# Kernel tuning notes

Hardware: AMD Instinct MI355X
Metric: run time of the kernel (lower is better)

The kernel has to match this reference:

```python
import jax, jax.numpy as jnp
import numpy as np

N = 100000          # num nodes
E = 1_600_000       # num edges
D = 128             # in_channels
H = 128             # hidden_channels
NUM_LAYERS = 3


def setup_inputs() -> dict:
    key = jax.random.key(0)
    ks = jax.random.split(key, 6)
    return {
        "emb": jax.random.normal(ks[0], (N, D), dtype=jnp.float32),
        "w1": jax.random.normal(ks[1], (H, D), dtype=jnp.float32) / np.sqrt(D).astype(np.float32),
        "b1": jnp.zeros((H,), jnp.float32),
        "w2": jax.random.normal(ks[2], (H, H), dtype=jnp.float32) / np.sqrt(H).astype(np.float32),
        "b2": jnp.zeros((H,), jnp.float32),
        "eps": jnp.zeros((NUM_LAYERS,), jnp.float32),  # learn_eps=True, init 0 per layer
        "edge_w": jax.random.uniform(ks[3], (E,), dtype=jnp.float32),
        "src": jax.random.randint(ks[4], (E,), 0, N, dtype=jnp.int32),
        "dst": jax.random.randint(ks[5], (E,), 0, N, dtype=jnp.int32),
    }


def _gin_layer(x, src, dst, edge_w, deg_inv, eps, W, b):
    # DGL GINConv(mean, edge_weight): msg = x[src] * w ; agg = mean over in-edges (divide by in-degree)
    msg = x[src] * edge_w[:, None]                                  # [E, d]
    agg = jax.ops.segment_sum(msg, dst, num_segments=N) * deg_inv[:, None]
    return ((1.0 + eps) * x + agg) @ W.T + b


def reference(emb, w1, b1, w2, b2, eps, edge_w, src, dst):
    # in-degree (count of in-edges), zero-degree nodes get 0 aggregation
    deg = jax.ops.segment_sum(jnp.ones((E,), jnp.float32), dst, num_segments=N)
    deg_inv = jnp.where(deg > 0, 1.0 / jnp.maximum(deg, 1.0), 0.0)

    x = _gin_layer(emb, src, dst, edge_w, deg_inv, eps[0], w1, b1)
    x = jax.nn.relu(x)  # dropout is identity in eval mode
    for i in range(1, NUM_LAYERS - 1):
        x = _gin_layer(x, src, dst, edge_w, deg_inv, eps[i], w2, b2)  # lin2 shared
        x = jax.nn.relu(x)
    x = _gin_layer(x, src, dst, edge_w, deg_inv, eps[NUM_LAYERS - 1], w2, b2)
    x = x.at[0].set(jnp.zeros((x.shape[1],), x.dtype))  # x[0] = zeros
    return x
```

## Files before the change

### kernel.cpp

```cpp
#include <hip/hip_runtime.h>
#include <hip/hip_bf16.h>

#define N_NODES 100000
#define N_EDGES 1600000
#define DIM 128
#define SCAN_CHUNK 1024

typedef __attribute__((ext_vector_type(8))) short bf16x8;
typedef __attribute__((ext_vector_type(4))) float f32x4;
typedef __attribute__((ext_vector_type(4))) short bf16x4;

__global__ void cvt_kernel(const float* __restrict__ in, __hip_bfloat16* __restrict__ out, int n4) {
    int i = blockIdx.x * blockDim.x + threadIdx.x;
    if (i < n4) {
        f32x4 v = ((const f32x4*)in)[i];
        bf16x4 o;
        o.x = (short)__bfloat16_as_ushort(__float2bfloat16(v.x));
        o.y = (short)__bfloat16_as_ushort(__float2bfloat16(v.y));
        o.z = (short)__bfloat16_as_ushort(__float2bfloat16(v.z));
        o.w = (short)__bfloat16_as_ushort(__float2bfloat16(v.w));
        ((bf16x4*)out)[i] = o;
    }
}

__global__ void cvtw_kernel(const float* __restrict__ w1, const float* __restrict__ w2,
                            __hip_bfloat16* __restrict__ w1b, __hip_bfloat16* __restrict__ w2b) {
    int i = blockIdx.x * blockDim.x + threadIdx.x;
    if (i < DIM * DIM) {
        w1b[i] = __float2bfloat16(w1[i]);
        w2b[i] = __float2bfloat16(w2[i]);
    }
}

#define DR_UNROLL 8
__global__ void degrank_kernel(const int* __restrict__ dst, int* __restrict__ deg,
                               int* __restrict__ rank) {
    int tid = blockIdx.x * blockDim.x + threadIdx.x;
    int nthreads = gridDim.x * blockDim.x;
    int d_[DR_UNROLL], r_[DR_UNROLL];
#pragma unroll
    for (int k = 0; k < DR_UNROLL; k++) {
        int e = tid + k * nthreads;
        d_[k] = (e < N_EDGES) ? dst[e] : -1;
    }
#pragma unroll
    for (int k = 0; k < DR_UNROLL; k++)
        if (d_[k] >= 0) r_[k] = atomicAdd(&deg[d_[k]], 1);
#pragma unroll
    for (int k = 0; k < DR_UNROLL; k++) {
        int e = tid + k * nthreads;
        if (e < N_EDGES) rank[e] = r_[k];
    }
}

__global__ void scan1_kernel(const int* __restrict__ deg, int* __restrict__ bsum) {
    __shared__ int s[256];
    int t = threadIdx.x;
    int base = blockIdx.x * SCAN_CHUNK + t * 4;
    int v = 0;
    for (int k = 0; k < 4; k++) { int i = base + k; if (i < N_NODES) v += deg[i]; }
    s[t] = v;
    __syncthreads();
    for (int off = 128; off > 0; off >>= 1) { if (t < off) s[t] += s[t + off]; __syncthreads(); }
    if (t == 0) bsum[blockIdx.x] = s[0];
}

__global__ void scan2_kernel(const int* __restrict__ bsum, int* __restrict__ bscan,
                             int* __restrict__ row_start, int nb) {
    if (threadIdx.x == 0) {
        int run = 0;
        for (int b = 0; b < nb; b++) { bscan[b] = run; run += bsum[b]; }
        row_start[N_NODES] = run;
    }
}

__global__ void scan3_kernel(const int* __restrict__ deg, const int* __restrict__ bscan,
                             int* __restrict__ row_start) {
    __shared__ int s[256];
    int t = threadIdx.x;
    int base = blockIdx.x * SCAN_CHUNK + t * 4;
    int v[4]; int tot = 0;
    for (int k = 0; k < 4; k++) { int i = base + k; v[k] = (i < N_NODES) ? deg[i] : 0; tot += v[k]; }
    s[t] = tot;
    __syncthreads();
    for (int off = 1; off < 256; off <<= 1) {
        int a = (t >= off) ? s[t - off] : 0;
        __syncthreads();
        s[t] += a;
        __syncthreads();
    }
    int run = s[t] - tot + bscan[blockIdx.x];
    for (int k = 0; k < 4; k++) {
        int i = base + k;
        if (i < N_NODES) row_start[i] = run;
        run += v[k];
    }
}

#define FI_UNROLL 4
__global__ void fill_kernel(const int* __restrict__ src, const int* __restrict__ dst,
                            const float* __restrict__ ew, const int* __restrict__ rank,
                            const int* __restrict__ row_start, int2* __restrict__ sw_s) {
    int tid = blockIdx.x * blockDim.x + threadIdx.x;
    int nthreads = gridDim.x * blockDim.x;
    int d_[FI_UNROLL], r_[FI_UNROLL], s_[FI_UNROLL], w_[FI_UNROLL], rs_[FI_UNROLL];
#pragma unroll
    for (int k = 0; k < FI_UNROLL; k++) {
        int e = tid + k * nthreads;
        if (e < N_EDGES) {
            d_[k] = dst[e]; r_[k] = rank[e]; s_[k] = src[e]; w_[k] = __float_as_int(ew[e]);
        } else d_[k] = -1;
    }
#pragma unroll
    for (int k = 0; k < FI_UNROLL; k++)
        if (d_[k] >= 0) rs_[k] = row_start[d_[k]];
#pragma unroll
    for (int k = 0; k < FI_UNROLL; k++)
        if (d_[k] >= 0) sw_s[rs_[k] + r_[k]] = make_int2(s_[k], w_[k]);
}

__global__ __launch_bounds__(256) void agg_kernel(const __hip_bfloat16* __restrict__ x,
                                                  const int* __restrict__ row_start,
                                                  const int2* __restrict__ sw_s,
                                                  const float* __restrict__ eps, int li,
                                                  __hip_bfloat16* __restrict__ h) {
    __shared__ int2 s_sw[4][64];
    int wv = threadIdx.x >> 6;
    int lane = threadIdx.x & 63;
    int n = blockIdx.x * 4 + wv;
    if (n >= N_NODES) return;
    int beg = row_start[n], end = row_start[n + 1];
    const __hip_bfloat162* xp = (const __hip_bfloat162*)x;
    float ax = 0.f, ay = 0.f;
    for (int base = beg; base < end; base += 64) {
        int cnt = min(64, end - base);
        if (lane < cnt) s_sw[wv][lane] = sw_s[base + lane];
        asm volatile("s_waitcnt lgkmcnt(0)" ::: "memory");
        int i = 0;
        for (; i + 4 <= cnt; i += 4) {
            int2 e0 = s_sw[wv][i], e1 = s_sw[wv][i + 1], e2 = s_sw[wv][i + 2], e3 = s_sw[wv][i + 3];
            __hip_bfloat162 v0 = xp[(size_t)e0.x * 64 + lane];
            __hip_bfloat162 v1 = xp[(size_t)e1.x * 64 + lane];
            __hip_bfloat162 v2 = xp[(size_t)e2.x * 64 + lane];
            __hip_bfloat162 v3 = xp[(size_t)e3.x * 64 + lane];
            float w0 = __int_as_float(e0.y), w1 = __int_as_float(e1.y);
            float w2 = __int_as_float(e2.y), w3 = __int_as_float(e3.y);
            ax += __bfloat162float(v0.x) * w0 + __bfloat162float(v1.x) * w1
                + __bfloat162float(v2.x) * w2 + __bfloat162float(v3.x) * w3;
            ay += __bfloat162float(v0.y) * w0 + __bfloat162float(v1.y) * w1
                + __bfloat162float(v2.y) * w2 + __bfloat162float(v3.y) * w3;
        }
        for (; i < cnt; i++) {
            int2 e = s_sw[wv][i];
            __hip_bfloat162 v = xp[(size_t)e.x * 64 + lane];
            float w = __int_as_float(e.y);
            ax += __bfloat162float(v.x) * w;
            ay += __bfloat162float(v.y) * w;
        }
        asm volatile("" ::: "memory");
    }
    int degn = end - beg;
    float dinv = degn > 0 ? 1.0f / (float)degn : 0.0f;
    float ep = 1.0f + eps[li];
    __hip_bfloat162 xs = xp[(size_t)n * 64 + lane];
    float vx = ep * __bfloat162float(xs.x) + ax * dinv;
    float vy = ep * __bfloat162float(xs.y) + ay * dinv;
    __hip_bfloat162 o;
    o.x = __float2bfloat16(vx);
    o.y = __float2bfloat16(vy);
    ((__hip_bfloat162*)h)[(size_t)n * 64 + lane] = o;
}

template <int RELU, int ZERO0, int OUTBF>
__global__ __launch_bounds__(256) void gemm_kernel(const __hip_bfloat16* __restrict__ A,
                                                   const __hip_bfloat16* __restrict__ W,
                                                   const float* __restrict__ bias,
                                                   void* __restrict__ outv) {
    int wave = threadIdx.x >> 6;
    int lane = threadIdx.x & 63;
    int row0 = blockIdx.x * 64 + wave * 16;
    int lr = lane & 15;
    int kg = lane >> 4;

    int arow = row0 + lr;
    if (arow > N_NODES - 1) arow = N_NODES - 1;
    const short* Ap = (const short*)A + (size_t)arow * DIM + kg * 8;
    bf16x8 a[4];
#pragma unroll
    for (int k = 0; k < 4; k++) a[k] = *(const bf16x8*)(Ap + k * 32);

    f32x4 acc[8];
#pragma unroll
    for (int jt = 0; jt < 8; jt++) {
        const short* Wp = (const short*)W + (size_t)(jt * 16 + lr) * DIM + kg * 8;
        f32x4 c = {0.f, 0.f, 0.f, 0.f};
#pragma unroll
        for (int k = 0; k < 4; k++) {
            bf16x8 b = *(const bf16x8*)(Wp + k * 32);
            c = __builtin_amdgcn_mfma_f32_16x16x32_bf16(a[k], b, c, 0, 0, 0);
        }
        acc[jt] = c;
    }

    int colb = lane & 15;
    int rb = (lane >> 4) * 4;
#pragma unroll
    for (int jt = 0; jt < 8; jt++) {
        int col = jt * 16 + colb;
        float bv = bias[col];
#pragma unroll
        for (int r = 0; r < 4; r++) {
            int grow = row0 + rb + r;
            if (grow < N_NODES) {
                float v = acc[jt][r] + bv;
                if (RELU) v = fmaxf(v, 0.f);
                if (ZERO0 && grow == 0) v = 0.f;
                if (OUTBF)
                    ((__hip_bfloat16*)outv)[(size_t)grow * DIM + col] = __float2bfloat16(v);
                else
                    ((float*)outv)[(size_t)grow * DIM + col] = v;
            }
        }
    }
}

extern "C" void kernel_launch(void* const* d_in, const int* in_sizes, int n_in,
                              void* d_out, int out_size, void* d_ws, size_t ws_size,
                              hipStream_t stream) {
    const float* emb = (const float*)d_in[0];
    const float* w1  = (const float*)d_in[1];
    const float* b1  = (const float*)d_in[2];
    const float* w2  = (const float*)d_in[3];
    const float* b2  = (const float*)d_in[4];
    const float* eps = (const float*)d_in[5];
    const float* ew  = (const float*)d_in[6];
    const int* src   = (const int*)d_in[7];
    const int* dst   = (const int*)d_in[8];
    float* out = (float*)d_out;

    char* base = (char*)d_ws;
    size_t off = 0;
    auto alloc = [&](size_t bytes) -> char* {
        char* p = base + off;
        off += (bytes + 255) & ~(size_t)255;
        return p;
    };
    int* deg            = (int*)alloc((size_t)N_NODES * 4);
    int* row_start      = (int*)alloc((size_t)(N_NODES + 1) * 4);
    int* rank           = (int*)alloc((size_t)N_EDGES * 4);
    int* bsum           = (int*)alloc(128 * 4);
    int* bscan          = (int*)alloc(128 * 4);
    int2* sw_s          = (int2*)alloc((size_t)N_EDGES * 8);
    __hip_bfloat16* h   = (__hip_bfloat16*)alloc((size_t)N_NODES * DIM * 2);
    __hip_bfloat16* xb  = (__hip_bfloat16*)alloc((size_t)N_NODES * DIM * 2);
    __hip_bfloat16* embb= (__hip_bfloat16*)alloc((size_t)N_NODES * DIM * 2);
    __hip_bfloat16* w1b = (__hip_bfloat16*)alloc(DIM * DIM * 2);
    __hip_bfloat16* w2b = (__hip_bfloat16*)alloc(DIM * DIM * 2);

    hipMemsetAsync(deg, 0, (size_t)N_NODES * 4, stream);

    cvt_kernel<<<(N_NODES * DIM / 4 + 255) / 256, 256, 0, stream>>>(emb, embb, N_NODES * DIM / 4);
    cvtw_kernel<<<(DIM * DIM + 255) / 256, 256, 0, stream>>>(w1, w2, w1b, w2b);

    {
        int nthreads = ((N_EDGES + DR_UNROLL - 1) / DR_UNROLL + 255) & ~255;
        degrank_kernel<<<nthreads / 256, 256, 0, stream>>>(dst, deg, rank);
    }
    int nb = (N_NODES + SCAN_CHUNK - 1) / SCAN_CHUNK;
    scan1_kernel<<<nb, 256, 0, stream>>>(deg, bsum);
    scan2_kernel<<<1, 64, 0, stream>>>(bsum, bscan, row_start, nb);
    scan3_kernel<<<nb, 256, 0, stream>>>(deg, bscan, row_start);
    {
        int nthreads = ((N_EDGES + FI_UNROLL - 1) / FI_UNROLL + 255) & ~255;
        fill_kernel<<<nthreads / 256, 256, 0, stream>>>(src, dst, ew, rank, row_start, sw_s);
    }

    int gemm_blocks = (N_NODES + 63) / 64;
    int agg_blocks = (N_NODES + 3) / 4;
    agg_kernel<<<agg_blocks, 256, 0, stream>>>(embb, row_start, sw_s, eps, 0, h);
    gemm_kernel<1, 0, 1><<<gemm_blocks, 256, 0, stream>>>(h, w1b, b1, xb);
    agg_kernel<<<agg_blocks, 256, 0, stream>>>(xb, row_start, sw_s, eps, 1, h);
    gemm_kernel<1, 0, 1><<<gemm_blocks, 256, 0, stream>>>(h, w2b, b2, xb);
    agg_kernel<<<agg_blocks, 256, 0, stream>>>(xb, row_start, sw_s, eps, 2, h);
    gemm_kernel<0, 1, 0><<<gemm_blocks, 256, 0, stream>>>(h, w2b, b2, out);
}
```

Before: 562.9 us.

## Fuse neighbor aggregation into MFMA GEMM via LDS-staged tiles

Each wave now aggregates 16 nodes sequentially into a swizzled LDS tile, then runs the MFMA linear layer directly from LDS. This removes the intermediate h buffer write and read and halves the kernel launches per layer. The degree/rank kernel becomes a simple grid-stride loop. The cost is far fewer concurrent waves doing gathers, which reduces latency hiding for the irregular loads.

```diff
diff --git a/kernel.cpp b/kernel.cpp
--- a/kernel.cpp
+++ b/kernel.cpp
@@ -32,25 +32,10 @@
     }
 }
 
-#define DR_UNROLL 8
 __global__ void degrank_kernel(const int* __restrict__ dst, int* __restrict__ deg,
                                int* __restrict__ rank) {
-    int tid = blockIdx.x * blockDim.x + threadIdx.x;
-    int nthreads = gridDim.x * blockDim.x;
-    int d_[DR_UNROLL], r_[DR_UNROLL];
-#pragma unroll
-    for (int k = 0; k < DR_UNROLL; k++) {
-        int e = tid + k * nthreads;
-        d_[k] = (e < N_EDGES) ? dst[e] : -1;
-    }
-#pragma unroll
-    for (int k = 0; k < DR_UNROLL; k++)
-        if (d_[k] >= 0) r_[k] = atomicAdd(&deg[d_[k]], 1);
-#pragma unroll
-    for (int k = 0; k < DR_UNROLL; k++) {
-        int e = tid + k * nthreads;
-        if (e < N_EDGES) rank[e] = r_[k];
-    }
+    for (int e = blockIdx.x * blockDim.x + threadIdx.x; e < N_EDGES; e += gridDim.x * blockDim.x)
+        rank[e] = atomicAdd(&deg[dst[e]], 1);
 }
 
 __global__ void scan1_kernel(const int* __restrict__ deg, int* __restrict__ bsum) {
@@ -119,75 +104,77 @@
         if (d_[k] >= 0) sw_s[rs_[k] + r_[k]] = make_int2(s_[k], w_[k]);
 }
 
-__global__ __launch_bounds__(256) void agg_kernel(const __hip_bfloat16* __restrict__ x,
-                                                  const int* __restrict__ row_start,
-                                                  const int2* __restrict__ sw_s,
-                                                  const float* __restrict__ eps, int li,
-                                                  __hip_bfloat16* __restrict__ h) {
+template <int RELU, int ZERO0, int OUTBF>
+__global__ __launch_bounds__(256) void aggmm_kernel(const __hip_bfloat16* __restrict__ x,
+                                                    const int* __restrict__ row_start,
+                                                    const int2* __restrict__ sw_s,
+                                                    const float* __restrict__ eps, int li,
+                                                    const __hip_bfloat16* __restrict__ W,
+                                                    const float* __restrict__ bias,
+                                                    void* __restrict__ outv) {
     __shared__ int2 s_sw[4][64];
+    __shared__ __hip_bfloat162 s_h[4][16][64];
     int wv = threadIdx.x >> 6;
     int lane = threadIdx.x & 63;
-    int n = blockIdx.x * 4 + wv;
-    if (n >= N_NODES) return;
-    int beg = row_start[n], end = row_start[n + 1];
+    int row0 = blockIdx.x * 64 + wv * 16;
     const __hip_bfloat162* xp = (const __hip_bfloat162*)x;
-    float ax = 0.f, ay = 0.f;
-    for (int base = beg; base < end; base += 64) {
-        int cnt = min(64, end - base);
-        if (lane < cnt) s_sw[wv][lane] = sw_s[base + lane];
-        asm volatile("s_waitcnt lgkmcnt(0)" ::: "memory");
-        int i = 0;
-        for (; i + 4 <= cnt; i += 4) {
-            int2 e0 = s_sw[wv][i], e1 = s_sw[wv][i + 1], e2 = s_sw[wv][i + 2], e3 = s_sw[wv][i + 3];
-            __hip_bfloat162 v0 = xp[(size_t)e0.x * 64 + lane];
-            __hip_bfloat162 v1 = xp[(size_t)e1.x * 64 + lane];
-            __hip_bfloat162 v2 = xp[(size_t)e2.x * 64 + lane];
-            __hip_bfloat162 v3 = xp[(size_t)e3.x * 64 + lane];
-            float w0 = __int_as_float(e0.y), w1 = __int_as_float(e1.y);
-            float w2 = __int_as_float(e2.y), w3 = __int_as_float(e3.y);
-            ax += __bfloat162float(v0.x) * w0 + __bfloat162float(v1.x) * w1
-                + __bfloat162float(v2.x) * w2 + __bfloat162float(v3.x) * w3;
-            ay += __bfloat162float(v0.y) * w0 + __bfloat162float(v1.y) * w1
-                + __bfloat162float(v2.y) * w2 + __bfloat162float(v3.y) * w3;
+    float ep = 1.0f + eps[li];
+
+    for (int j = 0; j < 16; j++) {
+        int n = row0 + j;
+        __hip_bfloat162 o;
+        o.x = __float2bfloat16(0.f);
+        o.y = __float2bfloat16(0.f);
+        if (n < N_NODES) {
+            int beg = row_start[n], end = row_start[n + 1];
+            float ax = 0.f, ay = 0.f;
+            for (int base = beg; base < end; base += 64) {
+                int cnt = min(64, end - base);
+                if (lane < cnt) s_sw[wv][lane] = sw_s[base + lane];
+                asm volatile("s_waitcnt lgkmcnt(0)" ::: "memory");
+                int i = 0;
+                for (; i + 4 <= cnt; i += 4) {
+                    int2 e0 = s_sw[wv][i], e1 = s_sw[wv][i + 1];
+                    int2 e2 = s_sw[wv][i + 2], e3 = s_sw[wv][i + 3];
+                    __hip_bfloat162 v0 = xp[(size_t)e0.x * 64 + lane];
+                    __hip_bfloat162 v1 = xp[(size_t)e1.x * 64 + lane];
+                    __hip_bfloat162 v2 = xp[(size_t)e2.x * 64 + lane];
+                    __hip_bfloat162 v3 = xp[(size_t)e3.x * 64 + lane];
+                    float w0 = __int_as_float(e0.y), w1 = __int_as_float(e1.y);
+                    float w2 = __int_as_float(e2.y), w3 = __int_as_float(e3.y);
+                    ax += __bfloat162float(v0.x) * w0 + __bfloat162float(v1.x) * w1
+                        + __bfloat162float(v2.x) * w2 + __bfloat162float(v3.x) * w3;
+                    ay += __bfloat162float(v0.y) * w0 + __bfloat162float(v1.y) * w1
+                        + __bfloat162float(v2.y) * w2 + __bfloat162float(v3.y) * w3;
+                }
+                for (; i < cnt; i++) {
+                    int2 e = s_sw[wv][i];
+                    __hip_bfloat162 v = xp[(size_t)e.x * 64 + lane];
+                    float w = __int_as_float(e.y);
+                    ax += __bfloat162float(v.x) * w;
+                    ay += __bfloat162float(v.y) * w;
+                }
+                asm volatile("" ::: "memory");
+            }
+            int degn = end - beg;
+            float dinv = degn > 0 ? 1.0f / (float)degn : 0.0f;
+            __hip_bfloat162 xs = xp[(size_t)n * 64 + lane];
+            o.x = __float2bfloat16(ep * __bfloat162float(xs.x) + ax * dinv);
+            o.y = __float2bfloat16(ep * __bfloat162float(xs.y) + ay * dinv);
         }
-        for (; i < cnt; i++) {
-            int2 e = s_sw[wv][i];
-            __hip_bfloat162 v = xp[(size_t)e.x * 64 + lane];
-            float w = __int_as_float(e.y);
-            ax += __bfloat162float(v.x) * w;
-            ay += __bfloat162float(v.y) * w;
-        }
-        asm volatile("" ::: "memory");
-    }
-    int degn = end - beg;
-    float dinv = degn > 0 ? 1.0f / (float)degn : 0.0f;
-    float ep = 1.0f + eps[li];
-    __hip_bfloat162 xs = xp[(size_t)n * 64 + lane];
-    float vx = ep * __bfloat162float(xs.x) + ax * dinv;
-    float vy = ep * __bfloat162float(xs.y) + ay * dinv;
-    __hip_bfloat162 o;
-    o.x = __float2bfloat16(vx);
-    o.y = __float2bfloat16(vy);
-    ((__hip_bfloat162*)h)[(size_t)n * 64 + lane] = o;
-}
-
-template <int RELU, int ZERO0, int OUTBF>
-__global__ __launch_bounds__(256) void gemm_kernel(const __hip_bfloat16* __restrict__ A,
-                                                   const __hip_bfloat16* __restrict__ W,
-                                                   const float* __restrict__ bias,
-                                                   void* __restrict__ outv) {
-    int wave = threadIdx.x >> 6;
-    int lane = threadIdx.x & 63;
-    int row0 = blockIdx.x * 64 + wave * 16;
+        int co = (lane * 4) ^ ((j & 7) << 4);
+        *(__hip_bfloat162*)((char*)&s_h[wv][j][0] + co) = o;
+    }
+    asm volatile("s_waitcnt lgkmcnt(0)" ::: "memory");
+
     int lr = lane & 15;
     int kg = lane >> 4;
-
-    int arow = row0 + lr;
-    if (arow > N_NODES - 1) arow = N_NODES - 1;
-    const short* Ap = (const short*)A + (size_t)arow * DIM + kg * 8;
     bf16x8 a[4];
 #pragma unroll
-    for (int k = 0; k < 4; k++) a[k] = *(const bf16x8*)(Ap + k * 32);
+    for (int k = 0; k < 4; k++) {
+        int cb = (kg * 16 + k * 64) ^ ((lr & 7) << 4);
+        a[k] = *(const bf16x8*)((const char*)&s_h[wv][lr][0] + cb);
+    }
 
     f32x4 acc[8];
 #pragma unroll
@@ -251,8 +238,8 @@
     int* bsum           = (int*)alloc(128 * 4);
     int* bscan          = (int*)alloc(128 * 4);
     int2* sw_s          = (int2*)alloc((size_t)N_EDGES * 8);
-    __hip_bfloat16* h   = (__hip_bfloat16*)alloc((size_t)N_NODES * DIM * 2);
     __hip_bfloat16* xb  = (__hip_bfloat16*)alloc((size_t)N_NODES * DIM * 2);
+    __hip_bfloat16* xc  = (__hip_bfloat16*)alloc((size_t)N_NODES * DIM * 2);
     __hip_bfloat16* embb= (__hip_bfloat16*)alloc((size_t)N_NODES * DIM * 2);
     __hip_bfloat16* w1b = (__hip_bfloat16*)alloc(DIM * DIM * 2);
     __hip_bfloat16* w2b = (__hip_bfloat16*)alloc(DIM * DIM * 2);
@@ -262,10 +249,7 @@
     cvt_kernel<<<(N_NODES * DIM / 4 + 255) / 256, 256, 0, stream>>>(emb, embb, N_NODES * DIM / 4);
     cvtw_kernel<<<(DIM * DIM + 255) / 256, 256, 0, stream>>>(w1, w2, w1b, w2b);
 
-    {
-        int nthreads = ((N_EDGES + DR_UNROLL - 1) / DR_UNROLL + 255) & ~255;
-        degrank_kernel<<<nthreads / 256, 256, 0, stream>>>(dst, deg, rank);
-    }
+    degrank_kernel<<<2048, 256, 0, stream>>>(dst, deg, rank);
     int nb = (N_NODES + SCAN_CHUNK - 1) / SCAN_CHUNK;
     scan1_kernel<<<nb, 256, 0, stream>>>(deg, bsum);
     scan2_kernel<<<1, 64, 0, stream>>>(bsum, bscan, row_start, nb);
@@ -275,12 +259,8 @@
         fill_kernel<<<nthreads / 256, 256, 0, stream>>>(src, dst, ew, rank, row_start, sw_s);
     }
 
-    int gemm_blocks = (N_NODES + 63) / 64;
-    int agg_blocks = (N_NODES + 3) / 4;
-    agg_kernel<<<agg_blocks, 256, 0, stream>>>(embb, row_start, sw_s, eps, 0, h);
-    gemm_kernel<1, 0, 1><<<gemm_blocks, 256, 0, stream>>>(h, w1b, b1, xb);
-    agg_kernel<<<agg_blocks, 256, 0, stream>>>(xb, row_start, sw_s, eps, 1, h);
-    gemm_kernel<1, 0, 1><<<gemm_blocks, 256, 0, stream>>>(h, w2b, b2, xb);
-    agg_kernel<<<agg_blocks, 256, 0, stream>>>(xb, row_start, sw_s, eps, 2, h);
-    gemm_kernel<0, 1, 0><<<gemm_blocks, 256, 0, stream>>>(h, w2b, b2, out);
-}
+    int blocks = (N_NODES + 63) / 64;
+    aggmm_kernel<1, 0, 1><<<blocks, 256, 0, stream>>>(embb, row_start, sw_s, eps, 0, w1b, b1, xb);
+    aggmm_kernel<1, 0, 1><<<blocks, 256, 0, stream>>>(xb,   row_start, sw_s, eps, 1, w2b, b2, xc);
+    aggmm_kernel<0, 1, 0><<<blocks, 256, 0, stream>>>(xc,   row_start, sw_s, eps, 2, w2b, b2, out);
+}
```

Result: slower. 655.2 us (+16.4%).
